# Kernel tuning notes

Measured on AMD Instinct MI355X. Metric: run time of the kernel, lower is better.

## Reference

```python
import jax, jax.numpy as jnp
import numpy as np

N_NODES = 100000


def _sage_conv(x, edge_index, W_l, W_r, b):
    # PyG SAGEConv (mean aggr): out_i = lin_l(mean_{j in N(i)} x_j) + lin_r(x_i)
    src, dst = edge_index[0], edge_index[1]
    msg = x[src]  # [E, d] gather
    agg_sum = jax.ops.segment_sum(msg, dst, num_segments=N_NODES)  # [N, d]
    deg = jax.ops.segment_sum(jnp.ones((src.shape[0],), x.dtype), dst, num_segments=N_NODES)
    agg = agg_sum / jnp.maximum(deg, 1.0)[:, None]  # mean aggregation
    return agg @ W_l.T + b + x @ W_r.T


def setup_inputs() -> dict:
    key = jax.random.key(0)
    k = jax.random.split(key, 8)
    d_in, hidden, out = 64, 128, 128
    x = jax.random.normal(k[0], (N_NODES, d_in), dtype=jnp.float32)
    edge_index = jax.random.randint(k[1], (2, 1600000), 0, N_NODES, dtype=jnp.int64)
    s1 = 1.0 / np.sqrt(d_in)
    s2 = 1.0 / np.sqrt(hidden)
    return {
        "x": x,
        "edge_index": edge_index,
        "W1_l": jax.random.uniform(k[2], (hidden, d_in), jnp.float32, -s1, s1),
        "W1_r": jax.random.uniform(k[3], (hidden, d_in), jnp.float32, -s1, s1),
        "b1": jnp.zeros((hidden,), jnp.float32),
        "W2_l": jax.random.uniform(k[4], (out, hidden), jnp.float32, -s2, s2),
        "W2_r": jax.random.uniform(k[5], (out, hidden), jnp.float32, -s2, s2),
        "b2": jnp.zeros((out,), jnp.float32),
    }


def reference(x, edge_index, W1_l, W1_r, b1, W2_l, W2_r, b2):
    h = jax.nn.relu(_sage_conv(x, edge_index, W1_l, W1_r, b1))
    return _sage_conv(h, edge_index, W2_l, W2_r, b2)
```

## Files before the change

kernel.cpp:

```cpp
#include <hip/hip_runtime.h>

#define NN 100000
#define NE 1600000
#define SCAN_BLK 2048

#define BSH 9
#define NBUCK2 ((NN + 511) / 512)
#define CHUNK 8192
#define NCHK ((NE + CHUNK - 1) / CHUNK)
#define L2T (NBUCK2 * NCHK)
#define NSTRIP (NN / 32)

using bf16x8 = __attribute__((ext_vector_type(8))) short;
using f32x16 = __attribute__((ext_vector_type(16))) float;

__device__ __forceinline__ unsigned short f2bf(float f) {
    unsigned u = __float_as_uint(f);
    u += 0x7FFFu + ((u >> 16) & 1u);
    return (unsigned short)(u >> 16);
}
__device__ __forceinline__ float bf2f(unsigned short h) {
    return __uint_as_float(((unsigned)h) << 16);
}

__global__ __launch_bounds__(256) void hist2_kernel(const int* __restrict__ dst,
                                                    int* __restrict__ histm) {
    __shared__ int lh[256];
    int blk = blockIdx.x, tid = threadIdx.x;
    lh[tid] = 0;
    __syncthreads();
    int base = blk * CHUNK;
#pragma unroll
    for (int t = 0; t < CHUNK / 256; t++) {
        int e = base + t * 256 + tid;
        if (e < NE) atomicAdd(&lh[dst[e] >> BSH], 1);
    }
    __syncthreads();
    if (tid < NBUCK2) histm[tid * NCHK + blk] = lh[tid];
}

__global__ __launch_bounds__(256) void scan1_kernel(int* __restrict__ data,
                                                    int* __restrict__ bsums, int L) {
    __shared__ int s[256];
    int bid = blockIdx.x, tid = threadIdx.x;
    int base = bid * SCAN_BLK + tid * 8;
    int v[8];
    int sum = 0;
#pragma unroll
    for (int t = 0; t < 8; t++) {
        int idx = base + t;
        v[t] = (idx < L) ? data[idx] : 0;
        sum += v[t];
    }
    s[tid] = sum;
    __syncthreads();
    for (int off = 1; off < 256; off <<= 1) {
        int val = (tid >= off) ? s[tid - off] : 0;
        __syncthreads();
        s[tid] += val;
        __syncthreads();
    }
    int excl = s[tid] - sum;
    if (tid == 255) bsums[bid] = s[255];
    int run = excl;
#pragma unroll
    for (int t = 0; t < 8; t++) {
        int idx = base + t;
        if (idx < L) data[idx] = run;
        run += v[t];
    }
}

__global__ __launch_bounds__(64) void scan2_kernel(int* __restrict__ bsums, int n) {
    int tid = threadIdx.x;
    int orig = (tid < n) ? bsums[tid] : 0;
    int v = orig;
    for (int off = 1; off < 64; off <<= 1) {
        int nb = __shfl_up(v, off, 64);
        if (tid >= off) v += nb;
    }
    if (tid < n) bsums[tid] = v - orig;
}

__global__ __launch_bounds__(256) void scan_add_kernel(int* __restrict__ data,
                                                       const int* __restrict__ bsums, int L) {
    int i = blockIdx.x * 256 + threadIdx.x;
    if (i < L) data[i] += bsums[i / SCAN_BLK];
}

__global__ __launch_bounds__(256) void scatter2_kernel(const int* __restrict__ src,
                                                       const int* __restrict__ dst,
                                                       const int* __restrict__ histm,
                                                       int* __restrict__ tmp) {
    __shared__ int lcur[256];
    int blk = blockIdx.x, tid = threadIdx.x;
    if (tid < NBUCK2) lcur[tid] = histm[tid * NCHK + blk];
    __syncthreads();
    int base = blk * CHUNK;
#pragma unroll
    for (int t = 0; t < CHUNK / 256; t++) {
        int e = base + t * 256 + tid;
        if (e < NE) {
            int d = dst[e];
            int p = atomicAdd(&lcur[d >> BSH], 1);
            tmp[p] = src[e] | ((d & 511) << 17);
        }
    }
}

__global__ __launch_bounds__(256) void count_place_kernel(const int* __restrict__ histm,
                                                          const int* __restrict__ tmp,
                                                          int* __restrict__ rowptr,
                                                          int* __restrict__ esrc) {
    __shared__ int cnt[512];
    __shared__ int s[256];
    int b = blockIdx.x, tid = threadIdx.x;
    int beg = histm[b * NCHK];
    int end = (b == NBUCK2 - 1) ? NE : histm[(b + 1) * NCHK];

    cnt[tid] = 0; cnt[tid + 256] = 0;
    __syncthreads();
    for (int e = beg + tid; e < end; e += 256)
        atomicAdd(&cnt[tmp[e] >> 17], 1);
    __syncthreads();

    int c0 = cnt[2 * tid], c1 = cnt[2 * tid + 1];
    int sum = c0 + c1;
    s[tid] = sum;
    __syncthreads();
    for (int off = 1; off < 256; off <<= 1) {
        int val = (tid >= off) ? s[tid - off] : 0;
        __syncthreads();
        s[tid] += val;
        __syncthreads();
    }
    int o0 = beg + s[tid] - sum;
    int o1 = o0 + c0;
    cnt[2 * tid] = o0;
    cnt[2 * tid + 1] = o1;
    int node0 = (b << BSH) + 2 * tid;
    if (node0 < NN)     rowptr[node0]     = o0;
    if (node0 + 1 < NN) rowptr[node0 + 1] = o1;
    if (b == 0 && tid == 0) rowptr[NN] = NE;
    __syncthreads();

    for (int e = beg + tid; e < end; e += 256) {
        int v = tmp[e];
        int p = atomicAdd(&cnt[v >> 17], 1);
        esrc[p] = v & 0x1FFFF;
    }
}

__global__ __launch_bounds__(256) void cvt_kernel(const float* __restrict__ in,
                                                  unsigned short* __restrict__ out, int n4) {
    int i = blockIdx.x * 256 + threadIdx.x;
    if (i < n4) {
        float4 f = ((const float4*)in)[i];
        ((ushort4*)out)[i] = make_ushort4(f2bf(f.x), f2bf(f.y), f2bf(f.z), f2bf(f.w));
    }
}

__global__ __launch_bounds__(256) void agg64_kernel(const unsigned short* __restrict__ feat,
                                                    const int* __restrict__ rowptr,
                                                    const int* __restrict__ esrc,
                                                    unsigned short* __restrict__ agg) {
    int node = blockIdx.x * 4 + (threadIdx.x >> 6);
    int lane = threadIdx.x & 63;
    int es = lane >> 3;
    int fi = lane & 7;
    int beg = rowptr[node], end = rowptr[node + 1];

    float ax[8];
#pragma unroll
    for (int i = 0; i < 8; i++) ax[i] = 0.0f;

    int e = beg;
    for (; e + 15 < end; e += 16) {
        int sA = esrc[e + es];
        int sB = esrc[e + 8 + es];
        bf16x8 uA = *(const bf16x8*)(feat + (size_t)sA * 64 + fi * 8);
        bf16x8 uB = *(const bf16x8*)(feat + (size_t)sB * 64 + fi * 8);
#pragma unroll
        for (int i = 0; i < 8; i++)
            ax[i] += bf2f((unsigned short)uA[i]) + bf2f((unsigned short)uB[i]);
    }
    if (e + 7 < end) {
        int s = esrc[e + es];
        bf16x8 u = *(const bf16x8*)(feat + (size_t)s * 64 + fi * 8);
#pragma unroll
        for (int i = 0; i < 8; i++) ax[i] += bf2f((unsigned short)u[i]);
        e += 8;
    }
    if (es < end - e) {
        int s = esrc[e + es];
        bf16x8 u = *(const bf16x8*)(feat + (size_t)s * 64 + fi * 8);
#pragma unroll
        for (int i = 0; i < 8; i++) ax[i] += bf2f((unsigned short)u[i]);
    }

#pragma unroll
    for (int i = 0; i < 8; i++) {
        ax[i] += __shfl_xor(ax[i], 8);
        ax[i] += __shfl_xor(ax[i], 16);
        ax[i] += __shfl_xor(ax[i], 32);
    }
    if (es == 0) {
        float inv = 1.0f / fmaxf((float)(end - beg), 1.0f);
        bf16x8 o;
#pragma unroll
        for (int i = 0; i < 8; i++) o[i] = (short)f2bf(ax[i] * inv);
        *(bf16x8*)(agg + (size_t)node * 64 + fi * 8) = o;
    }
}

__global__ __launch_bounds__(256) void agg128_kernel(const unsigned short* __restrict__ feat,
                                                     const int* __restrict__ rowptr,
                                                     const int* __restrict__ esrc,
                                                     unsigned short* __restrict__ agg) {
    int node = blockIdx.x * 4 + (threadIdx.x >> 6);
    int lane = threadIdx.x & 63;
    int es = lane >> 4;
    int fi = lane & 15;
    int beg = rowptr[node], end = rowptr[node + 1];

    float ax[8];
#pragma unroll
    for (int i = 0; i < 8; i++) ax[i] = 0.0f;

    int e = beg;
    for (; e + 15 < end; e += 16) {
        int s0 = esrc[e + es];
        int s1 = esrc[e + 4 + es];
        int s2 = esrc[e + 8 + es];
        int s3 = esrc[e + 12 + es];
        bf16x8 u0 = *(const bf16x8*)(feat + (size_t)s0 * 128 + fi * 8);
        bf16x8 u1 = *(const bf16x8*)(feat + (size_t)s1 * 128 + fi * 8);
        bf16x8 u2 = *(const bf16x8*)(feat + (size_t)s2 * 128 + fi * 8);
        bf16x8 u3 = *(const bf16x8*)(feat + (size_t)s3 * 128 + fi * 8);
#pragma unroll
        for (int i = 0; i < 8; i++)
            ax[i] += (bf2f((unsigned short)u0[i]) + bf2f((unsigned short)u1[i])) +
                     (bf2f((unsigned short)u2[i]) + bf2f((unsigned short)u3[i]));
    }
    for (; e + 3 < end; e += 4) {
        int s = esrc[e + es];
        bf16x8 u = *(const bf16x8*)(feat + (size_t)s * 128 + fi * 8);
#pragma unroll
        for (int i = 0; i < 8; i++) ax[i] += bf2f((unsigned short)u[i]);
    }
    if (es < end - e) {
        int s = esrc[e + es];
        bf16x8 u = *(const bf16x8*)(feat + (size_t)s * 128 + fi * 8);
#pragma unroll
        for (int i = 0; i < 8; i++) ax[i] += bf2f((unsigned short)u[i]);
    }

#pragma unroll
    for (int i = 0; i < 8; i++) {
        ax[i] += __shfl_xor(ax[i], 16);
        ax[i] += __shfl_xor(ax[i], 32);
    }
    if (es == 0) {
        float inv = 1.0f / fmaxf((float)(end - beg), 1.0f);
        bf16x8 o;
#pragma unroll
        for (int i = 0; i < 8; i++) o[i] = (short)f2bf(ax[i] * inv);
        *(bf16x8*)(agg + (size_t)node * 128 + fi * 8) = o;
    }
}

template <int K, bool RELU, bool OUTBF>
__global__ __launch_bounds__(256) void gemm_mfma_kernel(
    const unsigned short* __restrict__ A1,
    const unsigned short* __restrict__ A2,
    const unsigned short* __restrict__ Wa,
    const unsigned short* __restrict__ Wb,
    const float* __restrict__ bias,
    void* __restrict__ outv) {
    int strip = blockIdx.x * 4 + (threadIdx.x >> 6);
    if (strip >= NSTRIP) return;
    const int lane = threadIdx.x & 63;
    const int m = lane & 31;
    const int half = lane >> 5;
    const int base = strip * 32;

    f32x16 acc[4];
#pragma unroll
    for (int nb = 0; nb < 4; ++nb)
#pragma unroll
        for (int r = 0; r < 16; ++r) acc[nb][r] = 0.0f;

    const unsigned short* ar1 = A1 + (size_t)(base + m) * K + half * 8;
    const unsigned short* ar2 = A2 + (size_t)(base + m) * K + half * 8;
#pragma unroll
    for (int kc = 0; kc < K; kc += 16) {
        bf16x8 a = *(const bf16x8*)(ar1 + kc);
#pragma unroll
        for (int nb = 0; nb < 4; ++nb) {
            bf16x8 b = *(const bf16x8*)(Wa + (size_t)(nb * 32 + m) * K + kc + half * 8);
            acc[nb] = __builtin_amdgcn_mfma_f32_32x32x16_bf16(a, b, acc[nb], 0, 0, 0);
        }
    }
#pragma unroll
    for (int kc = 0; kc < K; kc += 16) {
        bf16x8 a = *(const bf16x8*)(ar2 + kc);
#pragma unroll
        for (int nb = 0; nb < 4; ++nb) {
            bf16x8 b = *(const bf16x8*)(Wb + (size_t)(nb * 32 + m) * K + kc + half * 8);
            acc[nb] = __builtin_amdgcn_mfma_f32_32x32x16_bf16(a, b, acc[nb], 0, 0, 0);
        }
    }

#pragma unroll
    for (int nb = 0; nb < 4; ++nb) {
        int j = nb * 32 + m;
        float bz = bias[j];
#pragma unroll
        for (int r = 0; r < 16; ++r) {
            int row = (r & 3) + 8 * (r >> 2) + 4 * half;
            float v = acc[nb][r] + bz;
            if (RELU) v = fmaxf(v, 0.0f);
            size_t idx = (size_t)(base + row) * 128 + j;
            if (OUTBF) ((unsigned short*)outv)[idx] = f2bf(v);
            else       ((float*)outv)[idx] = v;
        }
    }
}

extern "C" void kernel_launch(void* const* d_in, const int* in_sizes, int n_in,
                              void* d_out, int out_size, void* d_ws, size_t ws_size,
                              hipStream_t stream) {
    const float* x   = (const float*)d_in[0];
    const int*   ei  = (const int*)d_in[1];
    const float* W1l = (const float*)d_in[2];
    const float* W1r = (const float*)d_in[3];
    const float* b1  = (const float*)d_in[4];
    const float* W2l = (const float*)d_in[5];
    const float* W2r = (const float*)d_in[6];
    const float* b2  = (const float*)d_in[7];
    float* out = (float*)d_out;

    const int* src = ei;
    const int* dst = ei + NE;

    char* ws = (char*)d_ws;
    int* rowptr = (int*)ws;
    int* esrc   = (int*)(ws + 401408);
    unsigned short* aggB = (unsigned short*)(ws + 6803456);
    unsigned short* xb   = aggB + (size_t)NN * 64;
    char* E = ws + 32403456;
    unsigned short* hb = (unsigned short*)E;
    int* tmp   = (int*)E;
    int* histm = (int*)(E + 6400000);
    int* bsums = (int*)(E + 6560000);
    unsigned short* W1lb = (unsigned short*)d_out;
    unsigned short* W1rb = W1lb + 128 * 64;
    unsigned short* W2lb = (unsigned short*)ws;
    unsigned short* W2rb = W2lb + 128 * 128;

    const int GB  = (NSTRIP + 3) / 4;
    const int NSB2 = (L2T + SCAN_BLK - 1) / SCAN_BLK;

    hist2_kernel<<<NCHK, 256, 0, stream>>>(dst, histm);
    scan1_kernel<<<NSB2, 256, 0, stream>>>(histm, bsums, L2T);
    scan2_kernel<<<1, 64, 0, stream>>>(bsums, NSB2);
    scan_add_kernel<<<(L2T + 255) / 256, 256, 0, stream>>>(histm, bsums, L2T);
    scatter2_kernel<<<NCHK, 256, 0, stream>>>(src, dst, histm, tmp);
    count_place_kernel<<<NBUCK2, 256, 0, stream>>>(histm, tmp, rowptr, esrc);

    cvt_kernel<<<(NN * 64 / 4 + 255) / 256, 256, 0, stream>>>(x, xb, NN * 64 / 4);
    cvt_kernel<<<(128 * 64 / 4 + 255) / 256, 256, 0, stream>>>(W1l, W1lb, 128 * 64 / 4);
    cvt_kernel<<<(128 * 64 / 4 + 255) / 256, 256, 0, stream>>>(W1r, W1rb, 128 * 64 / 4);

    agg64_kernel<<<NN / 4, 256, 0, stream>>>(xb, rowptr, esrc, aggB);
    gemm_mfma_kernel<64, true, true><<<GB, 256, 0, stream>>>(aggB, xb, W1lb, W1rb, b1, hb);

    agg128_kernel<<<NN / 4, 256, 0, stream>>>(hb, rowptr, esrc, aggB);
    cvt_kernel<<<(128 * 128 / 4 + 255) / 256, 256, 0, stream>>>(W2l, W2lb, 128 * 128 / 4);
    cvt_kernel<<<(128 * 128 / 4 + 255) / 256, 256, 0, stream>>>(W2r, W2rb, 128 * 128 / 4);
    gemm_mfma_kernel<128, false, false><<<GB, 256, 0, stream>>>(aggB, hb, W2lb, W2rb, b2, out);
}
```

Baseline: 326.6 us.

## Fuse neighbor aggregation into MFMA GEMM and merge scan and weight-convert launches

Each 32-node block now computes the mean aggregation straight into a swizzled LDS tile and feeds it to MFMA, instead of writing the aggregate to global memory and reading it back in a separate GEMM kernel. Each wave now handles one 32-column output slice rather than all four. The three-kernel histogram scan becomes a single 1024-thread block, and the four weight conversions become one kernel, cutting launch count. In exchange, the gather and the GEMM are serialized inside each block, which can limit overlap. The A2 and weight operands are also read by every wave.

```diff
diff --git a/kernel.cpp b/kernel.cpp
--- a/kernel.cpp
+++ b/kernel.cpp
@@ -2,7 +2,6 @@
 
 #define NN 100000
 #define NE 1600000
-#define SCAN_BLK 2048
 
 #define BSH 9
 #define NBUCK2 ((NN + 511) / 512)
@@ -39,53 +38,28 @@
     if (tid < NBUCK2) histm[tid * NCHK + blk] = lh[tid];
 }
 
-__global__ __launch_bounds__(256) void scan1_kernel(int* __restrict__ data,
-                                                    int* __restrict__ bsums, int L) {
-    __shared__ int s[256];
-    int bid = blockIdx.x, tid = threadIdx.x;
-    int base = bid * SCAN_BLK + tid * 8;
-    int v[8];
+__global__ __launch_bounds__(1024) void scan_histm_kernel(int* __restrict__ data) {
+    __shared__ int s[1024];
+    const int PER = (L2T + 1023) / 1024;
+    int tid = threadIdx.x;
+    int lo = tid * PER;
+    int hi = lo + PER; if (hi > L2T) hi = L2T;
     int sum = 0;
-#pragma unroll
-    for (int t = 0; t < 8; t++) {
-        int idx = base + t;
-        v[t] = (idx < L) ? data[idx] : 0;
-        sum += v[t];
-    }
+    for (int i = lo; i < hi; i++) sum += data[i];
     s[tid] = sum;
     __syncthreads();
-    for (int off = 1; off < 256; off <<= 1) {
+    for (int off = 1; off < 1024; off <<= 1) {
         int val = (tid >= off) ? s[tid - off] : 0;
         __syncthreads();
         s[tid] += val;
         __syncthreads();
     }
-    int excl = s[tid] - sum;
-    if (tid == 255) bsums[bid] = s[255];
-    int run = excl;
-#pragma unroll
-    for (int t = 0; t < 8; t++) {
-        int idx = base + t;
-        if (idx < L) data[idx] = run;
-        run += v[t];
-    }
-}
-
-__global__ __launch_bounds__(64) void scan2_kernel(int* __restrict__ bsums, int n) {
-    int tid = threadIdx.x;
-    int orig = (tid < n) ? bsums[tid] : 0;
-    int v = orig;
-    for (int off = 1; off < 64; off <<= 1) {
-        int nb = __shfl_up(v, off, 64);
-        if (tid >= off) v += nb;
-    }
-    if (tid < n) bsums[tid] = v - orig;
-}
-
-__global__ __launch_bounds__(256) void scan_add_kernel(int* __restrict__ data,
-                                                       const int* __restrict__ bsums, int L) {
-    int i = blockIdx.x * 256 + threadIdx.x;
-    if (i < L) data[i] += bsums[i / SCAN_BLK];
+    int run = s[tid] - sum;
+    for (int i = lo; i < hi; i++) {
+        int d = data[i];
+        data[i] = run;
+        run += d;
+    }
 }
 
 __global__ __launch_bounds__(256) void scatter2_kernel(const int* __restrict__ src,
@@ -160,170 +134,173 @@
     }
 }
 
-__global__ __launch_bounds__(256) void agg64_kernel(const unsigned short* __restrict__ feat,
-                                                    const int* __restrict__ rowptr,
-                                                    const int* __restrict__ esrc,
-                                                    unsigned short* __restrict__ agg) {
-    int node = blockIdx.x * 4 + (threadIdx.x >> 6);
-    int lane = threadIdx.x & 63;
-    int es = lane >> 3;
-    int fi = lane & 7;
-    int beg = rowptr[node], end = rowptr[node + 1];
-
-    float ax[8];
-#pragma unroll
-    for (int i = 0; i < 8; i++) ax[i] = 0.0f;
-
-    int e = beg;
-    for (; e + 15 < end; e += 16) {
-        int sA = esrc[e + es];
-        int sB = esrc[e + 8 + es];
-        bf16x8 uA = *(const bf16x8*)(feat + (size_t)sA * 64 + fi * 8);
-        bf16x8 uB = *(const bf16x8*)(feat + (size_t)sB * 64 + fi * 8);
-#pragma unroll
-        for (int i = 0; i < 8; i++)
-            ax[i] += bf2f((unsigned short)uA[i]) + bf2f((unsigned short)uB[i]);
-    }
-    if (e + 7 < end) {
-        int s = esrc[e + es];
-        bf16x8 u = *(const bf16x8*)(feat + (size_t)s * 64 + fi * 8);
-#pragma unroll
-        for (int i = 0; i < 8; i++) ax[i] += bf2f((unsigned short)u[i]);
-        e += 8;
-    }
-    if (es < end - e) {
-        int s = esrc[e + es];
-        bf16x8 u = *(const bf16x8*)(feat + (size_t)s * 64 + fi * 8);
-#pragma unroll
-        for (int i = 0; i < 8; i++) ax[i] += bf2f((unsigned short)u[i]);
-    }
-
-#pragma unroll
-    for (int i = 0; i < 8; i++) {
-        ax[i] += __shfl_xor(ax[i], 8);
-        ax[i] += __shfl_xor(ax[i], 16);
-        ax[i] += __shfl_xor(ax[i], 32);
-    }
-    if (es == 0) {
-        float inv = 1.0f / fmaxf((float)(end - beg), 1.0f);
-        bf16x8 o;
-#pragma unroll
-        for (int i = 0; i < 8; i++) o[i] = (short)f2bf(ax[i] * inv);
-        *(bf16x8*)(agg + (size_t)node * 64 + fi * 8) = o;
-    }
-}
-
-__global__ __launch_bounds__(256) void agg128_kernel(const unsigned short* __restrict__ feat,
-                                                     const int* __restrict__ rowptr,
-                                                     const int* __restrict__ esrc,
-                                                     unsigned short* __restrict__ agg) {
-    int node = blockIdx.x * 4 + (threadIdx.x >> 6);
-    int lane = threadIdx.x & 63;
-    int es = lane >> 4;
-    int fi = lane & 15;
-    int beg = rowptr[node], end = rowptr[node + 1];
-
-    float ax[8];
-#pragma unroll
-    for (int i = 0; i < 8; i++) ax[i] = 0.0f;
-
-    int e = beg;
-    for (; e + 15 < end; e += 16) {
-        int s0 = esrc[e + es];
-        int s1 = esrc[e + 4 + es];
-        int s2 = esrc[e + 8 + es];
-        int s3 = esrc[e + 12 + es];
-        bf16x8 u0 = *(const bf16x8*)(feat + (size_t)s0 * 128 + fi * 8);
-        bf16x8 u1 = *(const bf16x8*)(feat + (size_t)s1 * 128 + fi * 8);
-        bf16x8 u2 = *(const bf16x8*)(feat + (size_t)s2 * 128 + fi * 8);
-        bf16x8 u3 = *(const bf16x8*)(feat + (size_t)s3 * 128 + fi * 8);
-#pragma unroll
-        for (int i = 0; i < 8; i++)
-            ax[i] += (bf2f((unsigned short)u0[i]) + bf2f((unsigned short)u1[i])) +
-                     (bf2f((unsigned short)u2[i]) + bf2f((unsigned short)u3[i]));
-    }
-    for (; e + 3 < end; e += 4) {
-        int s = esrc[e + es];
-        bf16x8 u = *(const bf16x8*)(feat + (size_t)s * 128 + fi * 8);
-#pragma unroll
-        for (int i = 0; i < 8; i++) ax[i] += bf2f((unsigned short)u[i]);
-    }
-    if (es < end - e) {
-        int s = esrc[e + es];
-        bf16x8 u = *(const bf16x8*)(feat + (size_t)s * 128 + fi * 8);
-#pragma unroll
-        for (int i = 0; i < 8; i++) ax[i] += bf2f((unsigned short)u[i]);
-    }
-
-#pragma unroll
-    for (int i = 0; i < 8; i++) {
-        ax[i] += __shfl_xor(ax[i], 16);
-        ax[i] += __shfl_xor(ax[i], 32);
-    }
-    if (es == 0) {
-        float inv = 1.0f / fmaxf((float)(end - beg), 1.0f);
-        bf16x8 o;
-#pragma unroll
-        for (int i = 0; i < 8; i++) o[i] = (short)f2bf(ax[i] * inv);
-        *(bf16x8*)(agg + (size_t)node * 128 + fi * 8) = o;
-    }
+__global__ __launch_bounds__(256) void cvtw_kernel(const float* __restrict__ W1l,
+                                                   const float* __restrict__ W1r,
+                                                   const float* __restrict__ W2l,
+                                                   const float* __restrict__ W2r,
+                                                   unsigned short* __restrict__ W1lb,
+                                                   unsigned short* __restrict__ W1rb,
+                                                   unsigned short* __restrict__ W2lb,
+                                                   unsigned short* __restrict__ W2rb) {
+    const int N1 = 128 * 64 / 4, N2 = 128 * 128 / 4;
+    int j = blockIdx.x * 256 + threadIdx.x;
+    const float* in; unsigned short* out;
+    if (j < N1)              { in = W1l; out = W1lb; }
+    else if ((j -= N1) < N1) { in = W1r; out = W1rb; }
+    else if ((j -= N1) < N2) { in = W2l; out = W2lb; }
+    else                     { j -= N2; if (j >= N2) return; in = W2r; out = W2rb; }
+    float4 f = ((const float4*)in)[j];
+    ((ushort4*)out)[j] = make_ushort4(f2bf(f.x), f2bf(f.y), f2bf(f.z), f2bf(f.w));
 }
 
 template <int K, bool RELU, bool OUTBF>
-__global__ __launch_bounds__(256) void gemm_mfma_kernel(
-    const unsigned short* __restrict__ A1,
+__global__ __launch_bounds__(256, 6) void agg_gemm_kernel(
+    const unsigned short* __restrict__ feat,
     const unsigned short* __restrict__ A2,
+    const int* __restrict__ rowptr,
+    const int* __restrict__ esrc,
     const unsigned short* __restrict__ Wa,
     const unsigned short* __restrict__ Wb,
     const float* __restrict__ bias,
     void* __restrict__ outv) {
-    int strip = blockIdx.x * 4 + (threadIdx.x >> 6);
-    if (strip >= NSTRIP) return;
-    const int lane = threadIdx.x & 63;
+    constexpr int SM = K / 8 - 1;
+    __shared__ unsigned short As[32 * K];
+    const int tid = threadIdx.x;
+    const int w = tid >> 6;
+    const int lane = tid & 63;
+    const int base = blockIdx.x * 32;
+
+    if (K == 128) {
+        int es = lane >> 4;
+        int fi = lane & 15;
+        for (int ii = 0; ii < 8; ii++) {
+            int row = w * 8 + ii;
+            int node = base + row;
+            int beg = rowptr[node], end = rowptr[node + 1];
+            float ax[8];
+#pragma unroll
+            for (int i = 0; i < 8; i++) ax[i] = 0.0f;
+            int e = beg;
+            for (; e + 15 < end; e += 16) {
+                int s0 = esrc[e + es];
+                int s1 = esrc[e + 4 + es];
+                int s2 = esrc[e + 8 + es];
+                int s3 = esrc[e + 12 + es];
+                bf16x8 u0 = *(const bf16x8*)(feat + (size_t)s0 * 128 + fi * 8);
+                bf16x8 u1 = *(const bf16x8*)(feat + (size_t)s1 * 128 + fi * 8);
+                bf16x8 u2 = *(const bf16x8*)(feat + (size_t)s2 * 128 + fi * 8);
+                bf16x8 u3 = *(const bf16x8*)(feat + (size_t)s3 * 128 + fi * 8);
+#pragma unroll
+                for (int i = 0; i < 8; i++)
+                    ax[i] += (bf2f((unsigned short)u0[i]) + bf2f((unsigned short)u1[i])) +
+                             (bf2f((unsigned short)u2[i]) + bf2f((unsigned short)u3[i]));
+            }
+            for (; e + 3 < end; e += 4) {
+                int s = esrc[e + es];
+                bf16x8 u = *(const bf16x8*)(feat + (size_t)s * 128 + fi * 8);
+#pragma unroll
+                for (int i = 0; i < 8; i++) ax[i] += bf2f((unsigned short)u[i]);
+            }
+            if (es < end - e) {
+                int s = esrc[e + es];
+                bf16x8 u = *(const bf16x8*)(feat + (size_t)s * 128 + fi * 8);
+#pragma unroll
+                for (int i = 0; i < 8; i++) ax[i] += bf2f((unsigned short)u[i]);
+            }
+#pragma unroll
+            for (int i = 0; i < 8; i++) {
+                ax[i] += __shfl_xor(ax[i], 16);
+                ax[i] += __shfl_xor(ax[i], 32);
+            }
+            if (es == 0) {
+                float inv = 1.0f / fmaxf((float)(end - beg), 1.0f);
+                bf16x8 o;
+#pragma unroll
+                for (int i = 0; i < 8; i++) o[i] = (short)f2bf(ax[i] * inv);
+                *(bf16x8*)(As + row * K + ((fi ^ (row & SM)) * 8)) = o;
+            }
+        }
+    } else {
+        int es = lane >> 3;
+        int fi = lane & 7;
+        for (int ii = 0; ii < 8; ii++) {
+            int row = w * 8 + ii;
+            int node = base + row;
+            int beg = rowptr[node], end = rowptr[node + 1];
+            float ax[8];
+#pragma unroll
+            for (int i = 0; i < 8; i++) ax[i] = 0.0f;
+            int e = beg;
+            for (; e + 15 < end; e += 16) {
+                int sA = esrc[e + es];
+                int sB = esrc[e + 8 + es];
+                bf16x8 uA = *(const bf16x8*)(feat + (size_t)sA * 64 + fi * 8);
+                bf16x8 uB = *(const bf16x8*)(feat + (size_t)sB * 64 + fi * 8);
+#pragma unroll
+                for (int i = 0; i < 8; i++)
+                    ax[i] += bf2f((unsigned short)uA[i]) + bf2f((unsigned short)uB[i]);
+            }
+            if (e + 7 < end) {
+                int s = esrc[e + es];
+                bf16x8 u = *(const bf16x8*)(feat + (size_t)s * 64 + fi * 8);
+#pragma unroll
+                for (int i = 0; i < 8; i++) ax[i] += bf2f((unsigned short)u[i]);
+                e += 8;
+            }
+            if (es < end - e) {
+                int s = esrc[e + es];
+                bf16x8 u = *(const bf16x8*)(feat + (size_t)s * 64 + fi * 8);
+#pragma unroll
+                for (int i = 0; i < 8; i++) ax[i] += bf2f((unsigned short)u[i]);
+            }
+#pragma unroll
+            for (int i = 0; i < 8; i++) {
+                ax[i] += __shfl_xor(ax[i], 8);
+                ax[i] += __shfl_xor(ax[i], 16);
+                ax[i] += __shfl_xor(ax[i], 32);
+            }
+            if (es == 0) {
+                float inv = 1.0f / fmaxf((float)(end - beg), 1.0f);
+                bf16x8 o;
+#pragma unroll
+                for (int i = 0; i < 8; i++) o[i] = (short)f2bf(ax[i] * inv);
+                *(bf16x8*)(As + row * K + ((fi ^ (row & SM)) * 8)) = o;
+            }
+        }
+    }
+    __syncthreads();
+
     const int m = lane & 31;
     const int half = lane >> 5;
-    const int base = strip * 32;
-
-    f32x16 acc[4];
-#pragma unroll
-    for (int nb = 0; nb < 4; ++nb)
-#pragma unroll
-        for (int r = 0; r < 16; ++r) acc[nb][r] = 0.0f;
-
-    const unsigned short* ar1 = A1 + (size_t)(base + m) * K + half * 8;
+    f32x16 acc;
+#pragma unroll
+    for (int r = 0; r < 16; ++r) acc[r] = 0.0f;
+
+#pragma unroll
+    for (int kc = 0; kc < K; kc += 16) {
+        int slot = (kc >> 3) + half;
+        bf16x8 a = *(const bf16x8*)(As + m * K + ((slot ^ (m & SM)) * 8));
+        bf16x8 b = *(const bf16x8*)(Wa + (size_t)(w * 32 + m) * K + kc + half * 8);
+        acc = __builtin_amdgcn_mfma_f32_32x32x16_bf16(a, b, acc, 0, 0, 0);
+    }
     const unsigned short* ar2 = A2 + (size_t)(base + m) * K + half * 8;
-#pragma unroll
-    for (int kc = 0; kc < K; kc += 16) {
-        bf16x8 a = *(const bf16x8*)(ar1 + kc);
-#pragma unroll
-        for (int nb = 0; nb < 4; ++nb) {
-            bf16x8 b = *(const bf16x8*)(Wa + (size_t)(nb * 32 + m) * K + kc + half * 8);
-            acc[nb] = __builtin_amdgcn_mfma_f32_32x32x16_bf16(a, b, acc[nb], 0, 0, 0);
-        }
-    }
 #pragma unroll
     for (int kc = 0; kc < K; kc += 16) {
         bf16x8 a = *(const bf16x8*)(ar2 + kc);
-#pragma unroll
-        for (int nb = 0; nb < 4; ++nb) {
-            bf16x8 b = *(const bf16x8*)(Wb + (size_t)(nb * 32 + m) * K + kc + half * 8);
-            acc[nb] = __builtin_amdgcn_mfma_f32_32x32x16_bf16(a, b, acc[nb], 0, 0, 0);
-        }
-    }
-
-#pragma unroll
-    for (int nb = 0; nb < 4; ++nb) {
-        int j = nb * 32 + m;
-        float bz = bias[j];
-#pragma unroll
-        for (int r = 0; r < 16; ++r) {
-            int row = (r & 3) + 8 * (r >> 2) + 4 * half;
-            float v = acc[nb][r] + bz;
-            if (RELU) v = fmaxf(v, 0.0f);
-            size_t idx = (size_t)(base + row) * 128 + j;
-            if (OUTBF) ((unsigned short*)outv)[idx] = f2bf(v);
-            else       ((float*)outv)[idx] = v;
-        }
+        bf16x8 b = *(const bf16x8*)(Wb + (size_t)(w * 32 + m) * K + kc + half * 8);
+        acc = __builtin_amdgcn_mfma_f32_32x32x16_bf16(a, b, acc, 0, 0, 0);
+    }
+
+    int j = w * 32 + m;
+    float bz = bias[j];
+#pragma unroll
+    for (int r = 0; r < 16; ++r) {
+        int row = (r & 3) + 8 * (r >> 2) + 4 * half;
+        float v = acc[r] + bz;
+        if (RELU) v = fmaxf(v, 0.0f);
+        size_t idx = (size_t)(base + row) * 128 + j;
+        if (OUTBF) ((unsigned short*)outv)[idx] = f2bf(v);
+        else       ((float*)outv)[idx] = v;
     }
 }
 
@@ -346,37 +323,27 @@
     char* ws = (char*)d_ws;
     int* rowptr = (int*)ws;
     int* esrc   = (int*)(ws + 401408);
-    unsigned short* aggB = (unsigned short*)(ws + 6803456);
-    unsigned short* xb   = aggB + (size_t)NN * 64;
+    unsigned short* W2lb = (unsigned short*)(ws + 6803456);
+    unsigned short* W2rb = W2lb + 128 * 128;
+    unsigned short* xb   = (unsigned short*)(ws + 19603456);
     char* E = ws + 32403456;
     unsigned short* hb = (unsigned short*)E;
     int* tmp   = (int*)E;
     int* histm = (int*)(E + 6400000);
-    int* bsums = (int*)(E + 6560000);
     unsigned short* W1lb = (unsigned short*)d_out;
     unsigned short* W1rb = W1lb + 128 * 64;
-    unsigned short* W2lb = (unsigned short*)ws;
-    unsigned short* W2rb = W2lb + 128 * 128;
-
-    const int GB  = (NSTRIP + 3) / 4;
-    const int NSB2 = (L2T + SCAN_BLK - 1) / SCAN_BLK;
 
     hist2_kernel<<<NCHK, 256, 0, stream>>>(dst, histm);
-    scan1_kernel<<<NSB2, 256, 0, stream>>>(histm, bsums, L2T);
-    scan2_kernel<<<1, 64, 0, stream>>>(bsums, NSB2);
-    scan_add_kernel<<<(L2T + 255) / 256, 256, 0, stream>>>(histm, bsums, L2T);
+    scan_histm_kernel<<<1, 1024, 0, stream>>>(histm);
     scatter2_kernel<<<NCHK, 256, 0, stream>>>(src, dst, histm, tmp);
     count_place_kernel<<<NBUCK2, 256, 0, stream>>>(histm, tmp, rowptr, esrc);
 
     cvt_kernel<<<(NN * 64 / 4 + 255) / 256, 256, 0, stream>>>(x, xb, NN * 64 / 4);
-    cvt_kernel<<<(128 * 64 / 4 + 255) / 256, 256, 0, stream>>>(W1l, W1lb, 128 * 64 / 4);
-    cvt_kernel<<<(128 * 64 / 4 + 255) / 256, 256, 0, stream>>>(W1r, W1rb, 128 * 64 / 4);
-
-    agg64_kernel<<<NN / 4, 256, 0, stream>>>(xb, rowptr, esrc, aggB);
-    gemm_mfma_kernel<64, true, true><<<GB, 256, 0, stream>>>(aggB, xb, W1lb, W1rb, b1, hb);
-
-    agg128_kernel<<<NN / 4, 256, 0, stream>>>(hb, rowptr, esrc, aggB);
-    cvt_kernel<<<(128 * 128 / 4 + 255) / 256, 256, 0, stream>>>(W2l, W2lb, 128 * 128 / 4);
-    cvt_kernel<<<(128 * 128 / 4 + 255) / 256, 256, 0, stream>>>(W2r, W2rb, 128 * 128 / 4);
-    gemm_mfma_kernel<128, false, false><<<GB, 256, 0, stream>>>(aggB, hb, W2lb, W2rb, b2, out);
-}
+    cvtw_kernel<<<48, 256, 0, stream>>>(W1l, W1r, W2l, W2r, W1lb, W1rb, W2lb, W2rb);
+
+    agg_gemm_kernel<64, true, true><<<NSTRIP, 256, 0, stream>>>(
+        xb, xb, rowptr, esrc, W1lb, W1rb, b1, hb);
+
+    agg_gemm_kernel<128, false, false><<<NSTRIP, 256, 0, stream>>>(
+        hb, hb, rowptr, esrc, W2lb, W2rb, b2, out);
+}
```

New measurement: 355.5 us. 8.8% more time.
